# Performance work log

Hardware: AMD Instinct MI355X
Metric: run time of the kernel (lower is better)

The kernel has to match this reference:

```python
import jax, jax.numpy as jnp
import numpy as np

D = 128  # input_dim

def setup_inputs() -> dict:
    key = jax.random.key(0)
    ks = jax.random.split(key, 9)
    B, Lq, Lkv = 4, 4096, 4096
    s = 1.0 / np.sqrt(D)
    return {
        "x1": jax.random.normal(ks[0], (B, Lq, D), dtype=jnp.float32),
        "x2": jax.random.normal(ks[1], (B, Lkv, D), dtype=jnp.float32),
        "x3": jax.random.normal(ks[2], (B, Lkv, D), dtype=jnp.float32),
        "Wq": jax.random.normal(ks[3], (D, D), dtype=jnp.float32) * s,
        "bq": jax.random.normal(ks[4], (D,), dtype=jnp.float32) * s,
        "Wk": jax.random.normal(ks[5], (D, D), dtype=jnp.float32) * s,
        "bk": jax.random.normal(ks[6], (D,), dtype=jnp.float32) * s,
        "Wv": jax.random.normal(ks[7], (D, D), dtype=jnp.float32) * s,
        "bv": jax.random.normal(ks[8], (D,), dtype=jnp.float32) * s,
    }

def reference(x1, x2, x3, Wq, bq, Wk, bk, Wv, bv):
    # torch Linear: y = x @ W.T + b
    q = jnp.einsum('bld,ed->ble', x1, Wq) + bq  # [B,Lq,D]
    k = jnp.einsum('bld,ed->ble', x2, Wk) + bk  # [B,Lkv,D]
    v = jnp.einsum('bld,ed->ble', x3, Wv) + bv  # [B,Lkv,D]
    scores = jnp.einsum('bqd,bkd->bqk', q, k) / jnp.sqrt(jnp.float32(x1.shape[-1]))
    attn = jax.nn.softmax(scores, axis=2)
    return jnp.einsum('bqk,bkd->bqd', attn, v)
```

## Files before the change

kernel.cpp:

```cpp
#include <hip/hip_runtime.h>
#include <hip/hip_bf16.h>

typedef __attribute__((ext_vector_type(8))) short short8;
typedef __attribute__((ext_vector_type(4))) float v4f;

__device__ __forceinline__ unsigned short f2bf(float f) {
    union { float f; unsigned u; } c; c.f = f;
    unsigned r = c.u + 0x7FFFu + ((c.u >> 16) & 1u);
    return (unsigned short)(r >> 16);
}
__device__ __forceinline__ unsigned pack2(float a, float b) {
    return (unsigned)f2bf(a) | ((unsigned)f2bf(b) << 16);
}
__device__ __forceinline__ float bf2f(unsigned short h) {
    union { unsigned u; float f; } c; c.u = ((unsigned)h) << 16;
    return c.f;
}

__device__ __forceinline__ void g2l16(const unsigned short* g, unsigned short* l) {
    __builtin_amdgcn_global_load_lds(
        (const __attribute__((address_space(1))) unsigned int*)g,
        (__attribute__((address_space(3))) unsigned int*)l,
        16, 0, 0);
}

__global__ __launch_bounds__(512) void proj_kernel(
    const float* __restrict__ x1, const float* __restrict__ x2, const float* __restrict__ x3,
    const float* __restrict__ Wq, const float* __restrict__ bq,
    const float* __restrict__ Wk, const float* __restrict__ bk,
    const float* __restrict__ Wv, const float* __restrict__ bv,
    unsigned short* __restrict__ qb, unsigned short* __restrict__ kb,
    unsigned short* __restrict__ vb, float qscale)
{
    __shared__ __attribute__((aligned(16))) unsigned short Xs[16384];
    __shared__ __attribute__((aligned(16))) unsigned short Ws[16384];

    int tid = threadIdx.x;
    int wave = tid >> 6, lane = tid & 63;
    int lmod = lane & 15, ldiv = lane >> 4;
    int p = blockIdx.x % 3;
    int row0 = (blockIdx.x / 3) * 128;

    const float* X = p == 0 ? x1 : p == 1 ? x2 : x3;
    const float* W = p == 0 ? Wq : p == 1 ? Wk : Wv;
    const float* bias = p == 0 ? bq : p == 1 ? bk : bv;
    float scale = p == 0 ? qscale : 1.0f;

#pragma unroll
    for (int i = 0; i < 8; i++) {
        int c = tid + i * 512;
        int row = c >> 5, d0 = (c & 31) * 4;
        v4f f = *(const v4f*)(X + (size_t)(row0 + row) * 128 + d0);
        int off = ((row >> 4) * 16 + (d0 >> 5) * 4 + ((d0 >> 3) & 3)) * 128 + (row & 15) * 8 + (d0 & 7);
        *(uint2*)&Xs[off] = make_uint2(pack2(f[0], f[1]), pack2(f[2], f[3]));
        v4f g = *(const v4f*)(W + (size_t)row * 128 + d0);
        *(uint2*)&Ws[off] = make_uint2(pack2(g[0], g[1]), pack2(g[2], g[3]));
    }
    __syncthreads();

    short8 af[4];
#pragma unroll
    for (int kc = 0; kc < 4; kc++)
        af[kc] = *(const short8*)&Xs[wave * 2048 + (kc * 4 + ldiv) * 128 + lmod * 8];

#pragma unroll
    for (int ct = 0; ct < 8; ct++) {
        v4f acc = {0.f, 0.f, 0.f, 0.f};
#pragma unroll
        for (int kc = 0; kc < 4; kc++) {
            short8 bf = *(const short8*)&Ws[ct * 2048 + (kc * 4 + ldiv) * 128 + lmod * 8];
            acc = __builtin_amdgcn_mfma_f32_16x16x32_bf16(af[kc], bf, acc, 0, 0, 0);
        }
        int e = ct * 16 + lmod;
        float bv_ = bias[e];
#pragma unroll
        for (int r = 0; r < 4; r++) {
            int orow = row0 + wave * 16 + ldiv * 4 + r;
            unsigned short h = f2bf((acc[r] + bv_) * scale);
            if (p == 0) {
                qb[(size_t)orow * 128 + e] = h;
            } else if (p == 1) {
                int b = orow >> 12, key = orow & 4095, kk = key & 31;
                kb[b * 524288 + (key >> 5) * 4096 + (kk & 1) * 2048
                   + ((e >> 5) * 4 + ((e >> 3) & 3)) * 128 + (kk >> 1) * 8 + (e & 7)] = h;
            } else {
                int b = orow >> 12, key = orow & 4095;
                vb[b * 524288 + (key >> 5) * 4096
                   + ((e >> 4) * 4 + ((key >> 3) & 3)) * 128 + (e & 15) * 8 + (key & 7)] = h;
            }
        }
    }
}

__global__ __launch_bounds__(256, 2) void attn_kernel(
    const unsigned short* __restrict__ Qb,
    const unsigned short* __restrict__ Kb,
    const unsigned short* __restrict__ Vb,
    unsigned short* __restrict__ Opart,
    float* __restrict__ Lbuf)
{
    __shared__ __attribute__((aligned(16))) unsigned short Kt[2][4096];
    __shared__ __attribute__((aligned(16))) unsigned short Vt[2][4096];
    __shared__ __attribute__((aligned(16))) unsigned short Ps[4][1280];

    int tid = threadIdx.x;
    int wave = tid >> 6, lane = tid & 63;
    int lmod = lane & 15, ldiv = lane >> 4;
    int split = blockIdx.x & 3;
    int qidx = blockIdx.x >> 2;
    int b = qidx >> 5;
    int q0 = (qidx & 31) * 128 + wave * 32;

    short8 qfrag[2][4];
#pragma unroll
    for (int set = 0; set < 2; set++) {
        const unsigned short* qptr = Qb + (size_t)(b * 4096 + q0 + set * 16 + lmod) * 128;
#pragma unroll
        for (int kc = 0; kc < 4; kc++)
            qfrag[set][kc] = *(const short8*)(qptr + kc * 32 + ldiv * 8);
    }

    v4f oacc[2][8];
#pragma unroll
    for (int set = 0; set < 2; set++)
#pragma unroll
        for (int dt = 0; dt < 8; dt++) oacc[set][dt] = (v4f){0.f, 0.f, 0.f, 0.f};
    float lsum[2][4] = {{0.f, 0.f, 0.f, 0.f}, {0.f, 0.f, 0.f, 0.f}};

    const unsigned short* kbase = Kb + b * 524288 + split * 131072;
    const unsigned short* vbase = Vb + b * 524288 + split * 131072;

#pragma unroll
    for (int i = 0; i < 2; i++) {
        g2l16(kbase + wave * 1024 + i * 512 + lane * 8, &Kt[0][wave * 1024 + i * 512]);
        g2l16(vbase + wave * 1024 + i * 512 + lane * 8, &Vt[0][wave * 1024 + i * 512]);
    }
    __syncthreads();

    for (int t = 0; t < 32; t++) {
        int cur = t & 1;
        if (t < 31) {
            const unsigned short* kg = kbase + (t + 1) * 4096;
            const unsigned short* vg = vbase + (t + 1) * 4096;
#pragma unroll
            for (int i = 0; i < 2; i++) {
                g2l16(kg + wave * 1024 + i * 512 + lane * 8, &Kt[cur ^ 1][wave * 1024 + i * 512]);
                g2l16(vg + wave * 1024 + i * 512 + lane * 8, &Vt[cur ^ 1][wave * 1024 + i * 512]);
            }
        }

        v4f sacc[2][2];
#pragma unroll
        for (int set = 0; set < 2; set++)
#pragma unroll
            for (int s = 0; s < 2; s++) sacc[set][s] = (v4f){0.f, 0.f, 0.f, 0.f};
#pragma unroll
        for (int kc = 0; kc < 4; kc++) {
            short8 kf0 = *(const short8*)&Kt[cur][(kc * 4 + ldiv) * 128 + lmod * 8];
            short8 kf1 = *(const short8*)&Kt[cur][2048 + (kc * 4 + ldiv) * 128 + lmod * 8];
            sacc[0][0] = __builtin_amdgcn_mfma_f32_16x16x32_bf16(qfrag[0][kc], kf0, sacc[0][0], 0, 0, 0);
            sacc[0][1] = __builtin_amdgcn_mfma_f32_16x16x32_bf16(qfrag[0][kc], kf1, sacc[0][1], 0, 0, 0);
            sacc[1][0] = __builtin_amdgcn_mfma_f32_16x16x32_bf16(qfrag[1][kc], kf0, sacc[1][0], 0, 0, 0);
            sacc[1][1] = __builtin_amdgcn_mfma_f32_16x16x32_bf16(qfrag[1][kc], kf1, sacc[1][1], 0, 0, 0);
        }

#pragma unroll
        for (int set = 0; set < 2; set++)
#pragma unroll
            for (int r = 0; r < 4; r++) {
                float p0 = __builtin_amdgcn_exp2f(sacc[set][0][r]);
                float p1 = __builtin_amdgcn_exp2f(sacc[set][1][r]);
                lsum[set][r] += p0 + p1;
                *(unsigned*)&Ps[wave][(set * 16 + 4 * ldiv + r) * 40 + lmod * 2] = pack2(p0, p1);
            }
        asm volatile("s_waitcnt lgkmcnt(0)" ::: "memory");

        short8 pf0 = *(const short8*)&Ps[wave][lmod * 40 + ldiv * 8];
        short8 pf1 = *(const short8*)&Ps[wave][(16 + lmod) * 40 + ldiv * 8];
#pragma unroll
        for (int dt = 0; dt < 8; dt++) {
            short8 vf = *(const short8*)&Vt[cur][(dt * 4 + ldiv) * 128 + lmod * 8];
            oacc[0][dt] = __builtin_amdgcn_mfma_f32_16x16x32_bf16(pf0, vf, oacc[0][dt], 0, 0, 0);
            oacc[1][dt] = __builtin_amdgcn_mfma_f32_16x16x32_bf16(pf1, vf, oacc[1][dt], 0, 0, 0);
        }
        __syncthreads();
    }

#pragma unroll
    for (int set = 0; set < 2; set++)
#pragma unroll
        for (int r = 0; r < 4; r++) {
            float lv = lsum[set][r];
            lv += __shfl_xor(lv, 1);
            lv += __shfl_xor(lv, 2);
            lv += __shfl_xor(lv, 4);
            lv += __shfl_xor(lv, 8);
            int gq = b * 4096 + q0 + set * 16 + 4 * ldiv + r;
            if (lmod == 0) Lbuf[split * 16384 + gq] = lv;
            unsigned short* obase = Opart + (size_t)(split * 16384 + gq) * 128;
#pragma unroll
            for (int dt = 0; dt < 8; dt++)
                obase[dt * 16 + lmod] = f2bf(oacc[set][dt][r]);
        }
}

__global__ __launch_bounds__(256) void merge_kernel(
    const unsigned short* __restrict__ Opart,
    const float* __restrict__ Lbuf,
    float* __restrict__ Out)
{
    int t = blockIdx.x * 256 + threadIdx.x;
#pragma unroll
    for (int it = 0; it < 4; it++) {
        int base = (t + it * 65536) * 8;
        int q = base >> 7;
        float inv = 1.0f / (Lbuf[q] + Lbuf[16384 + q] + Lbuf[32768 + q] + Lbuf[49152 + q]);
        float acc[8] = {0.f, 0.f, 0.f, 0.f, 0.f, 0.f, 0.f, 0.f};
#pragma unroll
        for (int s = 0; s < 4; s++) {
            short8 o = *(const short8*)(Opart + (size_t)s * 2097152 + base);
#pragma unroll
            for (int j = 0; j < 8; j++) acc[j] += bf2f((unsigned short)o[j]);
        }
        v4f lo = {acc[0] * inv, acc[1] * inv, acc[2] * inv, acc[3] * inv};
        v4f hi = {acc[4] * inv, acc[5] * inv, acc[6] * inv, acc[7] * inv};
        *(v4f*)(Out + base) = lo;
        *(v4f*)(Out + base + 4) = hi;
    }
}

extern "C" void kernel_launch(void* const* d_in, const int* in_sizes, int n_in,
                              void* d_out, int out_size, void* d_ws, size_t ws_size,
                              hipStream_t stream) {
    const float* x1 = (const float*)d_in[0];
    const float* x2 = (const float*)d_in[1];
    const float* x3 = (const float*)d_in[2];
    const float* Wq = (const float*)d_in[3];
    const float* bq = (const float*)d_in[4];
    const float* Wk = (const float*)d_in[5];
    const float* bk = (const float*)d_in[6];
    const float* Wv = (const float*)d_in[7];
    const float* bv = (const float*)d_in[8];
    float* out = (float*)d_out;

    unsigned short* qb = (unsigned short*)d_ws;
    unsigned short* kb = qb + (size_t)2097152;
    unsigned short* vb = kb + (size_t)2097152;
    unsigned short* op = vb + (size_t)2097152;
    float* lb = (float*)(op + (size_t)8388608);

    const float qscale = 1.4426950408889634f / 11.313708498984761f;

    proj_kernel<<<384, 512, 0, stream>>>(x1, x2, x3, Wq, bq, Wk, bk, Wv, bv,
                                         qb, kb, vb, qscale);
    attn_kernel<<<512, 256, 0, stream>>>(qb, kb, vb, op, lb);
    merge_kernel<<<256, 256, 0, stream>>>(op, lb, out);
}
```

Measured before the change: 141.9 us.

## Halve per-wave query tile in attention for higher occupancy, add setprio and pk-bf16 convert

The attention kernel now gives each wave 16 query rows instead of 32. This halves the accumulator registers, doubles the grid to 1024 blocks and raises launch bounds to 4 blocks per CU, with the P staging buffer shrunk to match. The intent is more concurrent waves to hide LDS and global latency. The cost is that each K/V tile loaded into LDS is reused across half as many queries, so K/V global traffic doubles. The change also wraps MFMA sections in s_setprio, replaces the software bf16 rounding with the v_cvt_pk_bf16_f32 instruction, and retunes the merge kernel grid.

Result: no change. 139.3 us (-1.8%).

```diff
diff --git a/kernel.cpp b/kernel.cpp
--- a/kernel.cpp
+++ b/kernel.cpp
@@ -9,8 +9,10 @@
     unsigned r = c.u + 0x7FFFu + ((c.u >> 16) & 1u);
     return (unsigned short)(r >> 16);
 }
-__device__ __forceinline__ unsigned pack2(float a, float b) {
-    return (unsigned)f2bf(a) | ((unsigned)f2bf(b) << 16);
+__device__ __forceinline__ unsigned cvtpk(float a, float b) {
+    unsigned r;
+    asm("v_cvt_pk_bf16_f32 %0, %1, %2" : "=v"(r) : "v"(a), "v"(b));
+    return r;
 }
 __device__ __forceinline__ float bf2f(unsigned short h) {
     union { unsigned u; float f; } c; c.u = ((unsigned)h) << 16;
@@ -52,9 +54,9 @@
         int row = c >> 5, d0 = (c & 31) * 4;
         v4f f = *(const v4f*)(X + (size_t)(row0 + row) * 128 + d0);
         int off = ((row >> 4) * 16 + (d0 >> 5) * 4 + ((d0 >> 3) & 3)) * 128 + (row & 15) * 8 + (d0 & 7);
-        *(uint2*)&Xs[off] = make_uint2(pack2(f[0], f[1]), pack2(f[2], f[3]));
+        *(uint2*)&Xs[off] = make_uint2(cvtpk(f[0], f[1]), cvtpk(f[2], f[3]));
         v4f g = *(const v4f*)(W + (size_t)row * 128 + d0);
-        *(uint2*)&Ws[off] = make_uint2(pack2(g[0], g[1]), pack2(g[2], g[3]));
+        *(uint2*)&Ws[off] = make_uint2(cvtpk(g[0], g[1]), cvtpk(g[2], g[3]));
     }
     __syncthreads();
 
@@ -92,7 +94,7 @@
     }
 }
 
-__global__ __launch_bounds__(256, 2) void attn_kernel(
+__global__ __launch_bounds__(256, 4) void attn_kernel(
     const unsigned short* __restrict__ Qb,
     const unsigned short* __restrict__ Kb,
     const unsigned short* __restrict__ Vb,
@@ -101,31 +103,28 @@
 {
     __shared__ __attribute__((aligned(16))) unsigned short Kt[2][4096];
     __shared__ __attribute__((aligned(16))) unsigned short Vt[2][4096];
-    __shared__ __attribute__((aligned(16))) unsigned short Ps[4][1280];
+    __shared__ __attribute__((aligned(16))) unsigned short Ps[4][640];
 
     int tid = threadIdx.x;
     int wave = tid >> 6, lane = tid & 63;
     int lmod = lane & 15, ldiv = lane >> 4;
     int split = blockIdx.x & 3;
     int qidx = blockIdx.x >> 2;
-    int b = qidx >> 5;
-    int q0 = (qidx & 31) * 128 + wave * 32;
-
-    short8 qfrag[2][4];
-#pragma unroll
-    for (int set = 0; set < 2; set++) {
-        const unsigned short* qptr = Qb + (size_t)(b * 4096 + q0 + set * 16 + lmod) * 128;
+    int b = qidx >> 6;
+    int q0 = (qidx & 63) * 64 + wave * 16;
+
+    short8 qfrag[4];
+    {
+        const unsigned short* qptr = Qb + (size_t)(b * 4096 + q0 + lmod) * 128;
 #pragma unroll
         for (int kc = 0; kc < 4; kc++)
-            qfrag[set][kc] = *(const short8*)(qptr + kc * 32 + ldiv * 8);
-    }
-
-    v4f oacc[2][8];
-#pragma unroll
-    for (int set = 0; set < 2; set++)
-#pragma unroll
-        for (int dt = 0; dt < 8; dt++) oacc[set][dt] = (v4f){0.f, 0.f, 0.f, 0.f};
-    float lsum[2][4] = {{0.f, 0.f, 0.f, 0.f}, {0.f, 0.f, 0.f, 0.f}};
+            qfrag[kc] = *(const short8*)(qptr + kc * 32 + ldiv * 8);
+    }
+
+    v4f oacc[8];
+#pragma unroll
+    for (int dt = 0; dt < 8; dt++) oacc[dt] = (v4f){0.f, 0.f, 0.f, 0.f};
+    float lsum[4] = {0.f, 0.f, 0.f, 0.f};
 
     const unsigned short* kbase = Kb + b * 524288 + split * 131072;
     const unsigned short* vbase = Vb + b * 524288 + split * 131072;
@@ -149,59 +148,53 @@
             }
         }
 
-        v4f sacc[2][2];
-#pragma unroll
-        for (int set = 0; set < 2; set++)
-#pragma unroll
-            for (int s = 0; s < 2; s++) sacc[set][s] = (v4f){0.f, 0.f, 0.f, 0.f};
+        v4f sacc[2];
+        sacc[0] = (v4f){0.f, 0.f, 0.f, 0.f};
+        sacc[1] = (v4f){0.f, 0.f, 0.f, 0.f};
+        __builtin_amdgcn_s_setprio(1);
 #pragma unroll
         for (int kc = 0; kc < 4; kc++) {
             short8 kf0 = *(const short8*)&Kt[cur][(kc * 4 + ldiv) * 128 + lmod * 8];
             short8 kf1 = *(const short8*)&Kt[cur][2048 + (kc * 4 + ldiv) * 128 + lmod * 8];
-            sacc[0][0] = __builtin_amdgcn_mfma_f32_16x16x32_bf16(qfrag[0][kc], kf0, sacc[0][0], 0, 0, 0);
-            sacc[0][1] = __builtin_amdgcn_mfma_f32_16x16x32_bf16(qfrag[0][kc], kf1, sacc[0][1], 0, 0, 0);
-            sacc[1][0] = __builtin_amdgcn_mfma_f32_16x16x32_bf16(qfrag[1][kc], kf0, sacc[1][0], 0, 0, 0);
-            sacc[1][1] = __builtin_amdgcn_mfma_f32_16x16x32_bf16(qfrag[1][kc], kf1, sacc[1][1], 0, 0, 0);
-        }
-
-#pragma unroll
-        for (int set = 0; set < 2; set++)
-#pragma unroll
-            for (int r = 0; r < 4; r++) {
-                float p0 = __builtin_amdgcn_exp2f(sacc[set][0][r]);
-                float p1 = __builtin_amdgcn_exp2f(sacc[set][1][r]);
-                lsum[set][r] += p0 + p1;
-                *(unsigned*)&Ps[wave][(set * 16 + 4 * ldiv + r) * 40 + lmod * 2] = pack2(p0, p1);
-            }
+            sacc[0] = __builtin_amdgcn_mfma_f32_16x16x32_bf16(qfrag[kc], kf0, sacc[0], 0, 0, 0);
+            sacc[1] = __builtin_amdgcn_mfma_f32_16x16x32_bf16(qfrag[kc], kf1, sacc[1], 0, 0, 0);
+        }
+        __builtin_amdgcn_s_setprio(0);
+
+#pragma unroll
+        for (int r = 0; r < 4; r++) {
+            float p0 = __builtin_amdgcn_exp2f(sacc[0][r]);
+            float p1 = __builtin_amdgcn_exp2f(sacc[1][r]);
+            lsum[r] += p0 + p1;
+            *(unsigned*)&Ps[wave][(4 * ldiv + r) * 40 + lmod * 2] = cvtpk(p0, p1);
+        }
         asm volatile("s_waitcnt lgkmcnt(0)" ::: "memory");
 
         short8 pf0 = *(const short8*)&Ps[wave][lmod * 40 + ldiv * 8];
-        short8 pf1 = *(const short8*)&Ps[wave][(16 + lmod) * 40 + ldiv * 8];
+        __builtin_amdgcn_s_setprio(1);
 #pragma unroll
         for (int dt = 0; dt < 8; dt++) {
             short8 vf = *(const short8*)&Vt[cur][(dt * 4 + ldiv) * 128 + lmod * 8];
-            oacc[0][dt] = __builtin_amdgcn_mfma_f32_16x16x32_bf16(pf0, vf, oacc[0][dt], 0, 0, 0);
-            oacc[1][dt] = __builtin_amdgcn_mfma_f32_16x16x32_bf16(pf1, vf, oacc[1][dt], 0, 0, 0);
-        }
+            oacc[dt] = __builtin_amdgcn_mfma_f32_16x16x32_bf16(pf0, vf, oacc[dt], 0, 0, 0);
+        }
+        __builtin_amdgcn_s_setprio(0);
         __syncthreads();
     }
 
 #pragma unroll
-    for (int set = 0; set < 2; set++)
-#pragma unroll
-        for (int r = 0; r < 4; r++) {
-            float lv = lsum[set][r];
-            lv += __shfl_xor(lv, 1);
-            lv += __shfl_xor(lv, 2);
-            lv += __shfl_xor(lv, 4);
-            lv += __shfl_xor(lv, 8);
-            int gq = b * 4096 + q0 + set * 16 + 4 * ldiv + r;
-            if (lmod == 0) Lbuf[split * 16384 + gq] = lv;
-            unsigned short* obase = Opart + (size_t)(split * 16384 + gq) * 128;
-#pragma unroll
-            for (int dt = 0; dt < 8; dt++)
-                obase[dt * 16 + lmod] = f2bf(oacc[set][dt][r]);
-        }
+    for (int r = 0; r < 4; r++) {
+        float lv = lsum[r];
+        lv += __shfl_xor(lv, 1);
+        lv += __shfl_xor(lv, 2);
+        lv += __shfl_xor(lv, 4);
+        lv += __shfl_xor(lv, 8);
+        int gq = b * 4096 + q0 + 4 * ldiv + r;
+        if (lmod == 0) Lbuf[split * 16384 + gq] = lv;
+        unsigned short* obase = Opart + (size_t)(split * 16384 + gq) * 128;
+#pragma unroll
+        for (int dt = 0; dt < 8; dt++)
+            obase[dt * 16 + lmod] = f2bf(oacc[dt][r]);
+    }
 }
 
 __global__ __launch_bounds__(256) void merge_kernel(
@@ -211,8 +204,8 @@
 {
     int t = blockIdx.x * 256 + threadIdx.x;
 #pragma unroll
-    for (int it = 0; it < 4; it++) {
-        int base = (t + it * 65536) * 8;
+    for (int it = 0; it < 2; it++) {
+        int base = (t + it * 131072) * 8;
         int q = base >> 7;
         float inv = 1.0f / (Lbuf[q] + Lbuf[16384 + q] + Lbuf[32768 + q] + Lbuf[49152 + q]);
         float acc[8] = {0.f, 0.f, 0.f, 0.f, 0.f, 0.f, 0.f, 0.f};
@@ -253,6 +246,6 @@
 
     proj_kernel<<<384, 512, 0, stream>>>(x1, x2, x3, Wq, bq, Wk, bk, Wv, bv,
                                          qb, kb, vb, qscale);
-    attn_kernel<<<512, 256, 0, stream>>>(qb, kb, vb, op, lb);
-    merge_kernel<<<256, 256, 0, stream>>>(op, lb, out);
-}
+    attn_kernel<<<1024, 256, 0, stream>>>(qb, kb, vb, op, lb);
+    merge_kernel<<<512, 256, 0, stream>>>(op, lb, out);
+}
```
